# Performance work log

Hardware: AMD Instinct MI355X
Metric: run time of the kernel (lower is better)

Reference implementation:

```python
import jax, jax.numpy as jnp
import numpy as np

N = 50000
E = 800000
IN_C = 128
HEADS = 2
OUT_C = 64
NEG_SLOPE = 0.2  # PyG GATConv leaky_relu slope


def setup_inputs() -> dict:
    key = jax.random.key(0)
    ks = jax.random.split(key, 12)
    glorot = lambda k, shape: jax.random.normal(k, shape, jnp.float32) * np.sqrt(2.0 / (shape[0] + shape[-1]))
    return {
        "node_h": jax.random.normal(ks[0], (N, IN_C), jnp.float32),
        "edge_index_pc": jax.random.randint(ks[1], (2, E), 0, N, jnp.int64),
        "edge_index_mc": jax.random.randint(ks[2], (2, E), 0, N, jnp.int64),
        "W_pc": glorot(ks[3], (IN_C, HEADS * OUT_C)),
        "att_src_pc": glorot(ks[4], (HEADS, OUT_C)),
        "att_dst_pc": glorot(ks[5], (HEADS, OUT_C)),
        "bias_pc": jnp.zeros((HEADS * OUT_C,), jnp.float32),
        "W_mc": glorot(ks[6], (IN_C, HEADS * OUT_C)),
        "att_src_mc": glorot(ks[7], (HEADS, OUT_C)),
        "att_dst_mc": glorot(ks[8], (HEADS, OUT_C)),
        "bias_mc": jnp.zeros((HEADS * OUT_C,), jnp.float32),
    }


def _gat_conv(x, edge_index, W, att_src, att_dst, bias):
    # PyG GATConv (concat=True). x: [N, in], edge_index: [2, E] (src -> dst).
    n = x.shape[0]
    H, C = att_src.shape
    xw = (x @ W).reshape(n, H, C)                      # [N, H, C]
    a_src = jnp.sum(xw * att_src, axis=-1)             # [N, H]
    a_dst = jnp.sum(xw * att_dst, axis=-1)             # [N, H]
    src, dst = edge_index[0], edge_index[1]
    e = jax.nn.leaky_relu(a_src[src] + a_dst[dst], negative_slope=NEG_SLOPE)  # [E, H]
    # segment softmax over edges sharing the same destination node
    m = jax.ops.segment_max(e, dst, num_segments=n)    # [N, H]
    m = jnp.where(jnp.isfinite(m), m, 0.0)             # guard isolated nodes
    ex = jnp.exp(e - m[dst])
    denom = jax.ops.segment_sum(ex, dst, num_segments=n)
    alpha = ex / (denom[dst] + 1e-16)                  # [E, H]
    msg = xw[src] * alpha[:, :, None]                  # [E, H, C]
    out = jax.ops.segment_sum(msg, dst, num_segments=n)  # [N, H, C]
    return out.reshape(n, H * C) + bias


def reference(node_h, edge_index_pc, edge_index_mc,
              W_pc, att_src_pc, att_dst_pc, bias_pc,
              W_mc, att_src_mc, att_dst_mc, bias_mc):
    # eval mode: F.dropout and GATConv attention dropout are identity
    h_pc = jax.nn.elu(_gat_conv(node_h, edge_index_pc, W_pc, att_src_pc, att_dst_pc, bias_pc))
    h_mc = jax.nn.elu(_gat_conv(node_h, edge_index_mc, W_mc, att_src_mc, att_dst_mc, bias_mc))
    return (h_pc + h_mc) * 0.5
```

## Files before the change

### kernel.cpp

```cpp
#include <hip/hip_runtime.h>
#include <hip/hip_bf16.h>

#define IN_C   128
#define HC     128
#define OUT_C  64
#define EPB    4096
#define NBMAX  1024
#define CAP    4096

typedef short bf16x8 __attribute__((ext_vector_type(8)));
typedef float f32x4  __attribute__((ext_vector_type(4)));

__device__ __forceinline__ unsigned short f2bf(float f) {
    unsigned u = __float_as_uint(f);
    return (unsigned short)((u + 0x7FFF + ((u >> 16) & 1)) >> 16);
}

__device__ __forceinline__ void fma8(float* acc, float al, uint4 v) {
    acc[0] += al * __uint_as_float(v.x << 16);
    acc[1] += al * __uint_as_float(v.x & 0xFFFF0000u);
    acc[2] += al * __uint_as_float(v.y << 16);
    acc[3] += al * __uint_as_float(v.y & 0xFFFF0000u);
    acc[4] += al * __uint_as_float(v.z << 16);
    acc[5] += al * __uint_as_float(v.z & 0xFFFF0000u);
// ... 12 lines not shown
        for (int k = 0; k < 512; ++k) {
            int ex = (u[k] >> 7) & 0xFF;
            if (ex >= 0xE0) { f32 = 1; break; }
        }
        flags[0] = f32;
        const int* a = (const int*)e1;
        const int* b = (const int*)e2;
        int any1 = 0, any2 = 0;
        for (int k = 0; k < 64; ++k) { any1 |= a[2*k+1]; any2 |= b[2*k+1]; }
        flags[1] = (any1 == 0);
        flags[2] = (any2 == 0);
        flags[3] = 0;
    }
}

__device__ __forceinline__ float ldf(const void* p, int i, int f32) {
    if (f32) return ((const float*)p)[i];
    return __bfloat162float(((const __hip_bfloat16*)p)[i]);
}

__device__ __forceinline__ void load_edge(const void* ei, int e, int E, int i64,
                                          int& s, int& d)
{
    if (i64) {
        s = (int)((const long long*)ei)[e];
        d = (int)((const long long*)ei)[E + e];
    } else {
        s = ((const int*)ei)[e];
        d = ((const int*)ei)[E + e];
    }
}

__global__ void k_fill_sentinel(float* out, int total, float v)
{
    int i = blockIdx.x * blockDim.x + threadIdx.x;
    if (i < total) out[i] = v;
}

__global__ __launch_bounds__(256)
void k_prep(const void* __restrict__ Wpc, const void* __restrict__ Wmc,
            const int* __restrict__ flags,
            unsigned short* __restrict__ WTpc, unsigned short* __restrict__ WTmc)
{
    int idx = blockIdx.x * 256 + threadIdx.x;
    if (idx >= 2 * IN_C * HC) return;
    int conv = idx >= IN_C * HC;
    int r = idx - conv * IN_C * HC;
    int k = r >> 7, j = r & 127;
    float v = ldf(conv ? Wmc : Wpc, r, flags[0]);
    (conv ? WTmc : WTpc)[(size_t)j * IN_C + k] = f2bf(v);
}

__global__ __launch_bounds__(256)
void k_gemm_mfma2(const void* __restrict__ h,
                  const unsigned short* __restrict__ WT0,
                  const unsigned short* __restrict__ WT1,
                  const void* __restrict__ atS0, const void* __restrict__ atD0,
                  const void* __restrict__ atS1, const void* __restrict__ atD1,
                  const int* __restrict__ flags,
                  unsigned short* __restrict__ xw0, unsigned short* __restrict__ xw1,
                  float* __restrict__ oas0, float* __restrict__ oad0,
                  float* __restrict__ oas1, float* __restrict__ oad1,
                  int n)
{
    int conv = blockIdx.y;
    const unsigned short* WT = conv ? WT1 : WT0;
    const void* atS = conv ? atS1 : atS0;
    const void* atD = conv ? atD1 : atD0;
    unsigned short* xw = conv ? xw1 : xw0;
    float* oaS = conv ? oas1 : oas0;
    float* oaD = conv ? oad1 : oad0;

    int tid = threadIdx.x;
    int wave = tid >> 6, lane = tid & 63;
    int cl = lane & 15, grp = lane >> 4;
    int base = blockIdx.x * 64 + wave * 16;
    int f32 = flags[0];

    int nodeLoad = base + cl;
    int nl = nodeLoad < n ? nodeLoad : (n - 1);
    bf16x8 afr[4];
    #pragma unroll
    for (int s = 0; s < 4; ++s) {
        int k0 = 32 * s + 8 * grp;
        if (f32) {
            const float4* hr = (const float4*)((const float*)h + (size_t)nl * IN_C + k0);
            float4 u0 = hr[0], u1 = hr[1];
            afr[s][0] = (short)f2bf(u0.x); afr[s][1] = (short)f2bf(u0.y);
            afr[s][2] = (short)f2bf(u0.z); afr[s][3] = (short)f2bf(u0.w);
            afr[s][4] = (short)f2bf(u1.x); afr[s][5] = (short)f2bf(u1.y);
            afr[s][6] = (short)f2bf(u1.z); afr[s][7] = (short)f2bf(u1.w);
        } else {
            afr[s] = *(const bf16x8*)((const unsigned short*)h + (size_t)nl * IN_C + k0);
        }
    }

    float vs_[4][2] = {{0.f,0.f},{0.f,0.f},{0.f,0.f},{0.f,0.f}};
    float vd_[4][2] = {{0.f,0.f},{0.f,0.f},{0.f,0.f},{0.f,0.f}};

    #pragma unroll
    for (int t = 0; t < 8; ++t) {
        int col = t * 16 + cl;
        f32x4 acc = {0.f, 0.f, 0.f, 0.f};
        #pragma unroll
        for (int s = 0; s < 4; ++s) {
            int k0 = 32 * s + 8 * grp;
            bf16x8 b = *(const bf16x8*)(WT + (size_t)col * IN_C + k0);
            acc = __builtin_amdgcn_mfma_f32_16x16x32_bf16(afr[s], b, acc, 0, 0, 0);
        }
        float aS = ldf(atS, col, f32);
        float aD = ldf(atD, col, f32);
        int hd = t >> 2;
        #pragma unroll
        for (int r = 0; r < 4; ++r) {
            int nodeOut = base + 4 * grp + r;
            float v = acc[r];
            if (nodeOut < n) xw[(size_t)nodeOut * HC + col] = f2bf(v);
            vs_[r][hd] += v * aS;
            vd_[r][hd] += v * aD;
        }
    }
    #pragma unroll
    for (int r = 0; r < 4; ++r) {
        #pragma unroll
        for (int hd = 0; hd < 2; ++hd) {
            float vs = vs_[r][hd], vd = vd_[r][hd];
            #pragma unroll
            for (int off = 1; off < 16; off <<= 1) {
                vs += __shfl_xor(vs, off);
                vd += __shfl_xor(vd, off);
            }
            int nodeOut = base + 4 * grp + r;
            if (cl == 0 && nodeOut < n) {
                oaS[nodeOut * 2 + hd] = vs;
                oaD[nodeOut * 2 + hd] = vd;
            }
        }
    }
}

__global__ __launch_bounds__(256)
void k_bscatter3(const void* __restrict__ e1, const void* __restrict__ e2, int E,
                 const int* __restrict__ flags, int NB,
                 int* __restrict__ gcur1, int* __restrict__ gcur2,
                 unsigned* __restrict__ bkt1, unsigned* __restrict__ bkt2)
{
    __shared__ int cnt[NBMAX];
    __shared__ int lbase[NBMAX];
    int conv = blockIdx.y;
    const void* ei = conv ? e2 : e1;
    int* gcur = conv ? gcur2 : gcur1;
    unsigned* bkt = conv ? bkt2 : bkt1;
    int tid = threadIdx.x;
    for (int i = tid; i < NB; i += 256) cnt[i] = 0;
    __syncthreads();
    int base = blockIdx.x * EPB;
    int i64 = flags[1 + conv];
    int ss[EPB / 256], dd[EPB / 256];
    #pragma unroll
    for (int k = 0; k < EPB / 256; ++k) {
        int e = base + k * 256 + tid;
        if (e < E) {
            int s, d; load_edge(ei, e, E, i64, s, d);
            ss[k] = s; dd[k] = d;
            atomicAdd(&cnt[d >> 7], 1);
        } else dd[k] = -1;
    }
    __syncthreads();
    for (int i = tid; i < NB; i += 256) {
        int c = cnt[i];
        lbase[i] = c ? atomicAdd(&gcur[i], c) : 0;
        cnt[i] = 0;
    }
    __syncthreads();
    #pragma unroll
    for (int k = 0; k < EPB / 256; ++k) {
        if (dd[k] >= 0) {
            int b = dd[k] >> 7;
            int pos = lbase[b] + atomicAdd(&cnt[b], 1);
            if (pos < CAP)
                bkt[(size_t)b * CAP + pos] =
                    ((unsigned)(dd[k] & 127) << 17) | (unsigned)ss[k];
        }
    }
}

__global__ __launch_bounds__(256)
void k_bcsr3(unsigned* __restrict__ bkt1, unsigned* __restrict__ bkt2,
             const int* __restrict__ gcur1, const int* __restrict__ gcur2,
             int2* __restrict__ rs1, int2* __restrict__ rs2,
             int NB, int n)
{
    __shared__ unsigned ebuf[CAP];
    __shared__ int cnt[128], off[128], exc[128];
    int conv = blockIdx.y;
    unsigned* seg = (conv ? bkt2 : bkt1) + (size_t)blockIdx.x * CAP;
    const int* gcur = conv ? gcur2 : gcur1;
    int2* rs = conv ? rs2 : rs1;
    int b = blockIdx.x, tid = threadIdx.x;
    int nb0 = b << 7;
    int nd = n - nb0; if (nd > 128) nd = 128;
    int cntE = gcur[b]; if (cntE > CAP) cntE = CAP;

    for (int i = tid; i < cntE; i += 256) ebuf[i] = seg[i];
    if (tid < 128) cnt[tid] = 0;
    __syncthreads();
    for (int i = tid; i < cntE; i += 256)
        atomicAdd(&cnt[ebuf[i] >> 17], 1);
    __syncthreads();
    int v = (tid < 128) ? cnt[tid] : 0;
    if (tid < 128) off[tid] = v;
    __syncthreads();
    for (int o = 1; o < 128; o <<= 1) {
        int x = (tid < 128 && tid >= o) ? off[tid - o] : 0;
        __syncthreads();
        if (tid < 128) off[tid] += x;
        __syncthreads();
    }
    if (tid < 128) exc[tid] = off[tid] - v;
    if (tid < nd) {
        int begA = b * CAP + exc[tid];
        rs[nb0 + tid] = make_int2(begA, begA + v);
    }
    if (tid < 128) cnt[tid] = 0;
    __syncthreads();
    for (int i = tid; i < cntE; i += 256) {
        unsigned pv = ebuf[i];
        int d = pv >> 17;
        int pos = atomicAdd(&cnt[d], 1);
        seg[exc[d] + pos] = pv & 0x1FFFFu;
    }
}

__global__ __launch_bounds__(256)
void k_node8(const int2* __restrict__ rs1, const int2* __restrict__ rs2,
             const unsigned* __restrict__ csr1, const unsigned* __restrict__ csr2,
             const float* __restrict__ as1, const float* __restrict__ ad1,
             const float* __restrict__ as2, const float* __restrict__ ad2,
             const unsigned short* __restrict__ xw1, const unsigned short* __restrict__ xw2,
             const void* __restrict__ bias1, const void* __restrict__ bias2,
             const int* __restrict__ flags,
             float* __restrict__ out, int n)
{
    __shared__ int   slds[16][66];
    __shared__ float e0l[16][66];
    __shared__ float e1l[16][66];
    int tid = threadIdx.x;
    int nl = tid >> 4;
    int l  = tid & 15;
    int node = blockIdx.x * 16 + nl;
    if (node >= n) return;
    int f32 = flags[0];
    unsigned lofs = (unsigned)(l << 4);
    int c0 = l * 8;
    float vv0[8];

    #pragma unroll
    for (int conv = 0; conv < 2; ++conv) {
        const int2* rs = conv ? rs2 : rs1;
        const unsigned* csr = conv ? csr2 : csr1;
        const float2* asv = (const float2*)(conv ? as2 : as1);
        const float2* adv = (const float2*)(conv ? ad2 : ad1);
        const char* xwb = (const char*)(conv ? xw2 : xw1);
        const void* bias = conv ? bias2 : bias1;

        int2 r = rs[node];
        int beg = r.x, end = r.y;
        int deg = end - beg;
        float2 ad = adv[node];

        float m0 = -1e30f, m1 = -1e30f;
        for (int f = l; f < deg; f += 16) {
            int src = (int)csr[beg + f];
            float2 as = asv[src];
            float e0 = as.x + ad.x; e0 = e0 > 0.f ? e0 : 0.2f * e0;
            float e1 = as.y + ad.y; e1 = e1 > 0.f ? e1 : 0.2f * e1;
            if (f < 64) { slds[nl][f] = src; e0l[nl][f] = e0; e1l[nl][f] = e1; }
            m0 = fmaxf(m0, e0); m1 = fmaxf(m1, e1);
        }
        #pragma unroll
        for (int off = 8; off; off >>= 1) {
            m0 = fmaxf(m0, __shfl_xor(m0, off));
            m1 = fmaxf(m1, __shfl_xor(m1, off));
        }

        float s0 = 0.f, s1 = 0.f;
        for (int f = l; f < deg; f += 16) {
            float ex0, ex1;
            if (f < 64) {
                ex0 = expf(e0l[nl][f] - m0);
                ex1 = expf(e1l[nl][f] - m1);
                e0l[nl][f] = ex0; e1l[nl][f] = ex1;
            } else {
                int src = (int)csr[beg + f];
                float2 as = asv[src];
                float e0 = as.x + ad.x; e0 = e0 > 0.f ? e0 : 0.2f * e0;
                float e1 = as.y + ad.y; e1 = e1 > 0.f ? e1 : 0.2f * e1;
                ex0 = expf(e0 - m0); ex1 = expf(e1 - m1);
            }
            s0 += ex0; s1 += ex1;
        }
        #pragma unroll
        for (int off = 8; off; off >>= 1) {
            s0 += __shfl_xor(s0, off);
            s1 += __shfl_xor(s1, off);
        }
        float inv = (l < 8) ? 1.f / (s0 + 1e-16f) : 1.f / (s1 + 1e-16f);
        float mh  = (l < 8) ? m0 : m1;

        float acc[8] = {0.f,0.f,0.f,0.f,0.f,0.f,0.f,0.f};
        int tcap = deg < 64 ? deg : 64;
        int t = 0;
        for (; t + 4 <= tcap; t += 4) {
            int sA = slds[nl][t],   sB = slds[nl][t+1];
            int sC = slds[nl][t+2], sD = slds[nl][t+3];
            float aA = (l < 8) ? e0l[nl][t]   : e1l[nl][t];
            float aB = (l < 8) ? e0l[nl][t+1] : e1l[nl][t+1];
            float aC = (l < 8) ? e0l[nl][t+2] : e1l[nl][t+2];
            float aD = (l < 8) ? e0l[nl][t+3] : e1l[nl][t+3];
            uint4 vA = *(const uint4*)(xwb + (((unsigned)sA) << 8) + lofs);
            uint4 vB = *(const uint4*)(xwb + (((unsigned)sB) << 8) + lofs);
            uint4 vC = *(const uint4*)(xwb + (((unsigned)sC) << 8) + lofs);
            uint4 vD = *(const uint4*)(xwb + (((unsigned)sD) << 8) + lofs);
            fma8(acc, aA * inv, vA);
            fma8(acc, aB * inv, vB);
            fma8(acc, aC * inv, vC);
            fma8(acc, aD * inv, vD);
        }
        for (; t < tcap; ++t) {
            int src = slds[nl][t];
            float exv = (l < 8) ? e0l[nl][t] : e1l[nl][t];
            uint4 v = *(const uint4*)(xwb + (((unsigned)src) << 8) + lofs);
            fma8(acc, exv * inv, v);
        }
        for (; t < deg; ++t) {
            int src = (int)csr[beg + t];
            float2 as = asv[src];
            float e = (l < 8) ? (as.x + ad.x) : (as.y + ad.y);
            e = e > 0.f ? e : 0.2f * e;
            float exv = expf(e - mh);
            uint4 v = *(const uint4*)(xwb + (((unsigned)src) << 8) + lofs);
            fma8(acc, exv * inv, v);
        }

        if (conv == 0) {
            #pragma unroll
            for (int j = 0; j < 8; ++j) {
                float v = acc[j] + ldf(bias, c0 + j, f32);
                vv0[j] = v > 0.f ? v : expf(v) - 1.f;
            }
        } else {
            float vv1[8];
            #pragma unroll
            for (int j = 0; j < 8; ++j) {
                float v = acc[j] + ldf(bias, c0 + j, f32);
                vv1[j] = v > 0.f ? v : expf(v) - 1.f;
            }
            float4* o4 = (float4*)(out + (size_t)node * HC + c0);
            o4[0] = make_float4(0.5f * (vv0[0] + vv1[0]), 0.5f * (vv0[1] + vv1[1]),
                                0.5f * (vv0[2] + vv1[2]), 0.5f * (vv0[3] + vv1[3]));
            o4[1] = make_float4(0.5f * (vv0[4] + vv1[4]), 0.5f * (vv0[5] + vv1[5]),
                                0.5f * (vv0[6] + vv1[6]), 0.5f * (vv0[7] + vv1[7]));
        }
    }
}

static inline char* align64(char* p) {
    return (char*)(((size_t)p + 63) & ~(size_t)63);
}

extern "C" void kernel_launch(void* const* d_in, const int* in_sizes, int n_in,
                              void* d_out, int out_size, void* d_ws, size_t ws_size,
                              hipStream_t stream)
{
    const void* node_h = d_in[0];
    const void* ei_pc  = d_in[1];
    const void* ei_mc  = d_in[2];
    const void* W_pc   = d_in[3];
    const void* as_pc  = d_in[4];
    const void* ad_pc  = d_in[5];
    const void* b_pc   = d_in[6];
    const void* W_mc   = d_in[7];
    const void* as_mc  = d_in[8];
    const void* ad_mc  = d_in[9];
    const void* b_mc   = d_in[10];

    const int N = in_sizes[0] / IN_C;
    const int E = in_sizes[1] / 2;
    const int total = N * HC;
    const int NB = (N + 127) >> 7;
    float* out = (float*)d_out;
    const int fillBlocks = (out_size + 255) / 256;

    char* p = (char*)d_ws;
    int* flags = (int*)p;                       p += 256;
    unsigned short* WT_pc = (unsigned short*)p; p += (size_t)IN_C * HC * 2;
    unsigned short* WT_mc = (unsigned short*)p; p += (size_t)IN_C * HC * 2;
    unsigned short* xw_pc = (unsigned short*)p; p += (size_t)total * 2;
    unsigned short* xw_mc = (unsigned short*)p; p += (size_t)total * 2;
    float* aspc = (float*)p;                    p += (size_t)N * 2 * 4;
    float* adpc = (float*)p;                    p += (size_t)N * 2 * 4;
    float* asmc = (float*)p;                    p += (size_t)N * 2 * 4;
    float* admc = (float*)p;                    p += (size_t)N * 2 * 4;
    char* zbase = p;
    int* gcur1 = (int*)p;                       p += (size_t)NBMAX * 4;
    int* gcur2 = (int*)p;                       p += (size_t)NBMAX * 4;
    size_t zbytes = (size_t)(p - zbase);
    p = align64(p);
    int2* rs1 = (int2*)p;                       p += (size_t)N * 8;  p = align64(p);
    int2* rs2 = (int2*)p;                       p += (size_t)N * 8;  p = align64(p);
    unsigned* bkt1 = (unsigned*)p;              p += (size_t)NB * CAP * 4;
    unsigned* bkt2 = (unsigned*)p;              p += (size_t)NB * CAP * 4;

    {
        float sentinel = 0.f;
        if (n_in < 11) sentinel = 690.f;
        else if (in_sizes[1] != in_sizes[2]) sentinel = 702.f;
        else if (in_sizes[3] != IN_C * HC)   sentinel = 703.f;
        else if (in_sizes[7] != IN_C * HC)   sentinel = 707.f;
        else if (out_size != total)          sentinel = 720.f;
        else if (NB > NBMAX)                 sentinel = 730.f;
        else if (N >= (1 << 17))             sentinel = 741.f;
        size_t need = (size_t)(p - (char*)d_ws);
        if (sentinel == 0.f && ws_size < need) sentinel = 555.f;
        if (sentinel != 0.f) {
            k_fill_sentinel<<<fillBlocks, 256, 0, stream>>>(out, out_size, sentinel);
            return;
        }
    }

    k_detect<<<1, 64, 0, stream>>>(node_h, ei_pc, ei_mc, flags);
    k_prep<<<(2 * IN_C * HC + 255) / 256, 256, 0, stream>>>(W_pc, W_mc, flags, WT_pc, WT_mc);
    hipMemsetAsync(zbase, 0, zbytes, stream);

    const int blocksB = (E + EPB - 1) / EPB;
    const int blocksN = (N + 15) / 16;
    const int blocksG = (N + 63) / 64;

    k_gemm_mfma2<<<dim3(blocksG, 2), 256, 0, stream>>>(node_h, WT_pc, WT_mc,
                                                       as_pc, ad_pc, as_mc, ad_mc, flags,
                                                       xw_pc, xw_mc, aspc, adpc, asmc, admc, N);

    k_bscatter3<<<dim3(blocksB, 2), 256, 0, stream>>>(ei_pc, ei_mc, E, flags, NB,
                                                      gcur1, gcur2, bkt1, bkt2);
    k_bcsr3<<<dim3(NB, 2), 256, 0, stream>>>(bkt1, bkt2, gcur1, gcur2, rs1, rs2, NB, N);

    k_node8<<<blocksN, 256, 0, stream>>>(rs1, rs2, bkt1, bkt2,
                                         aspc, adpc, asmc, admc,
                                         xw_pc, xw_mc, b_pc, b_mc, flags,
                                         out, N);
}
```

Measured before the change: 156.9 us.

## Merge GEMM and edge bucket scatter into one launch; interleave both convs in aggregation

```diff
diff --git a/kernel.cpp b/kernel.cpp
--- a/kernel.cpp
+++ b/kernel.cpp
@@ -88,135 +88,137 @@
 }
 
 __global__ __launch_bounds__(256)
-void k_gemm_mfma2(const void* __restrict__ h,
-                  const unsigned short* __restrict__ WT0,
-                  const unsigned short* __restrict__ WT1,
-                  const void* __restrict__ atS0, const void* __restrict__ atD0,
-                  const void* __restrict__ atS1, const void* __restrict__ atD1,
-                  const int* __restrict__ flags,
-                  unsigned short* __restrict__ xw0, unsigned short* __restrict__ xw1,
-                  float* __restrict__ oas0, float* __restrict__ oad0,
-                  float* __restrict__ oas1, float* __restrict__ oad1,
-                  int n)
-{
-    int conv = blockIdx.y;
-    const unsigned short* WT = conv ? WT1 : WT0;
-    const void* atS = conv ? atS1 : atS0;
-    const void* atD = conv ? atD1 : atD0;
-    unsigned short* xw = conv ? xw1 : xw0;
-    float* oaS = conv ? oas1 : oas0;
-    float* oaD = conv ? oad1 : oad0;
-
+void k_gs(const void* __restrict__ h,
+          const unsigned short* __restrict__ WT0,
+          const unsigned short* __restrict__ WT1,
+          const void* __restrict__ atS0, const void* __restrict__ atD0,
+          const void* __restrict__ atS1, const void* __restrict__ atD1,
+          const int* __restrict__ flags,
+          unsigned short* __restrict__ xw0, unsigned short* __restrict__ xw1,
+          float* __restrict__ oas0, float* __restrict__ oad0,
+          float* __restrict__ oas1, float* __restrict__ oad1,
+          int n, int blocksG,
+          const void* __restrict__ e1, const void* __restrict__ e2, int E,
+          int NB, int blocksB,
+          int* __restrict__ gcur1, int* __restrict__ gcur2,
+          unsigned* __restrict__ bkt1, unsigned* __restrict__ bkt2)
+{
+    __shared__ int sh[2 * NBMAX];
     int tid = threadIdx.x;
-    int wave = tid >> 6, lane = tid & 63;
-    int cl = lane & 15, grp = lane >> 4;
-    int base = blockIdx.x * 64 + wave * 16;
-    int f32 = flags[0];
-
-    int nodeLoad = base + cl;
-    int nl = nodeLoad < n ? nodeLoad : (n - 1);
-    bf16x8 afr[4];
-    #pragma unroll
-    for (int s = 0; s < 4; ++s) {
-        int k0 = 32 * s + 8 * grp;
-        if (f32) {
-            const float4* hr = (const float4*)((const float*)h + (size_t)nl * IN_C + k0);
-            float4 u0 = hr[0], u1 = hr[1];
-            afr[s][0] = (short)f2bf(u0.x); afr[s][1] = (short)f2bf(u0.y);
-            afr[s][2] = (short)f2bf(u0.z); afr[s][3] = (short)f2bf(u0.w);
-            afr[s][4] = (short)f2bf(u1.x); afr[s][5] = (short)f2bf(u1.y);
-            afr[s][6] = (short)f2bf(u1.z); afr[s][7] = (short)f2bf(u1.w);
-        } else {
-            afr[s] = *(const bf16x8*)((const unsigned short*)h + (size_t)nl * IN_C + k0);
-        }
-    }
-
-    float vs_[4][2] = {{0.f,0.f},{0.f,0.f},{0.f,0.f},{0.f,0.f}};
-    float vd_[4][2] = {{0.f,0.f},{0.f,0.f},{0.f,0.f},{0.f,0.f}};
-
-    #pragma unroll
-    for (int t = 0; t < 8; ++t) {
-        int col = t * 16 + cl;
-        f32x4 acc = {0.f, 0.f, 0.f, 0.f};
+
+    if (blockIdx.y < 2) {
+        if ((int)blockIdx.x >= blocksG) return;
+        int conv = blockIdx.y;
+        const unsigned short* WT = conv ? WT1 : WT0;
+        const void* atS = conv ? atS1 : atS0;
+        const void* atD = conv ? atD1 : atD0;
+        unsigned short* xw = conv ? xw1 : xw0;
+        float* oaS = conv ? oas1 : oas0;
+        float* oaD = conv ? oad1 : oad0;
+
+        int wave = tid >> 6, lane = tid & 63;
+        int cl = lane & 15, grp = lane >> 4;
+        int base = blockIdx.x * 64 + wave * 16;
+        int f32 = flags[0];
+
+        int nodeLoad = base + cl;
+        int nl = nodeLoad < n ? nodeLoad : (n - 1);
+        bf16x8 afr[4];
         #pragma unroll
         for (int s = 0; s < 4; ++s) {
             int k0 = 32 * s + 8 * grp;
-            bf16x8 b = *(const bf16x8*)(WT + (size_t)col * IN_C + k0);
-            acc = __builtin_amdgcn_mfma_f32_16x16x32_bf16(afr[s], b, acc, 0, 0, 0);
-        }
-        float aS = ldf(atS, col, f32);
-        float aD = ldf(atD, col, f32);
-        int hd = t >> 2;
+            if (f32) {
+                const float4* hr = (const float4*)((const float*)h + (size_t)nl * IN_C + k0);
+                float4 u0 = hr[0], u1 = hr[1];
+                afr[s][0] = (short)f2bf(u0.x); afr[s][1] = (short)f2bf(u0.y);
+                afr[s][2] = (short)f2bf(u0.z); afr[s][3] = (short)f2bf(u0.w);
+                afr[s][4] = (short)f2bf(u1.x); afr[s][5] = (short)f2bf(u1.y);
+                afr[s][6] = (short)f2bf(u1.z); afr[s][7] = (short)f2bf(u1.w);
+            } else {
+                afr[s] = *(const bf16x8*)((const unsigned short*)h + (size_t)nl * IN_C + k0);
+            }
+        }
+
+        float vs_[4][2] = {{0.f,0.f},{0.f,0.f},{0.f,0.f},{0.f,0.f}};
+        float vd_[4][2] = {{0.f,0.f},{0.f,0.f},{0.f,0.f},{0.f,0.f}};
+
+        #pragma unroll
+        for (int t = 0; t < 8; ++t) {
+            int col = t * 16 + cl;
+            f32x4 acc = {0.f, 0.f, 0.f, 0.f};
+            #pragma unroll
+            for (int s = 0; s < 4; ++s) {
+                int k0 = 32 * s + 8 * grp;
+                bf16x8 b = *(const bf16x8*)(WT + (size_t)col * IN_C + k0);
+                acc = __builtin_amdgcn_mfma_f32_16x16x32_bf16(afr[s], b, acc, 0, 0, 0);
+            }
+            float aS = ldf(atS, col, f32);
+            float aD = ldf(atD, col, f32);
+            int hd = t >> 2;
+            #pragma unroll
+            for (int r = 0; r < 4; ++r) {
+                int nodeOut = base + 4 * grp + r;
+                float v = acc[r];
+                if (nodeOut < n) xw[(size_t)nodeOut * HC + col] = f2bf(v);
+                vs_[r][hd] += v * aS;
+                vd_[r][hd] += v * aD;
+            }
+        }
         #pragma unroll
         for (int r = 0; r < 4; ++r) {
-            int nodeOut = base + 4 * grp + r;
-            float v = acc[r];
-            if (nodeOut < n) xw[(size_t)nodeOut * HC + col] = f2bf(v);
-            vs_[r][hd] += v * aS;
-            vd_[r][hd] += v * aD;
-        }
-    }
-    #pragma unroll
-    for (int r = 0; r < 4; ++r) {
+            #pragma unroll
+            for (int hd = 0; hd < 2; ++hd) {
+                float vs = vs_[r][hd], vd = vd_[r][hd];
+                #pragma unroll
+                for (int off = 1; off < 16; off <<= 1) {
+                    vs += __shfl_xor(vs, off);
+                    vd += __shfl_xor(vd, off);
+                }
+                int nodeOut = base + 4 * grp + r;
+                if (cl == 0 && nodeOut < n) {
+                    oaS[nodeOut * 2 + hd] = vs;
+                    oaD[nodeOut * 2 + hd] = vd;
+                }
+            }
+        }
+    } else {
+        if ((int)blockIdx.x >= blocksB) return;
+        int conv = blockIdx.y - 2;
+        const void* ei = conv ? e2 : e1;
+        int* gcur = conv ? gcur2 : gcur1;
+        unsigned* bkt = conv ? bkt2 : bkt1;
+        int* cnt = sh;
+        int* lbase = sh + NBMAX;
+        for (int i = tid; i < NB; i += 256) cnt[i] = 0;
+        __syncthreads();
+        int base = blockIdx.x * EPB;
+        int i64 = flags[1 + conv];
+        int ss[EPB / 256], dd[EPB / 256];
         #pragma unroll
-        for (int hd = 0; hd < 2; ++hd) {
-            float vs = vs_[r][hd], vd = vd_[r][hd];
-            #pragma unroll
-            for (int off = 1; off < 16; off <<= 1) {
-                vs += __shfl_xor(vs, off);
-                vd += __shfl_xor(vd, off);
+        for (int k = 0; k < EPB / 256; ++k) {
+            int e = base + k * 256 + tid;
+            if (e < E) {
+                int s, d; load_edge(ei, e, E, i64, s, d);
+                ss[k] = s; dd[k] = d;
+                atomicAdd(&cnt[d >> 7], 1);
+            } else dd[k] = -1;
+        }
+        __syncthreads();
+        for (int i = tid; i < NB; i += 256) {
+            int c = cnt[i];
+            lbase[i] = c ? atomicAdd(&gcur[i], c) : 0;
+            cnt[i] = 0;
+        }
+        __syncthreads();
+        #pragma unroll
+        for (int k = 0; k < EPB / 256; ++k) {
+            if (dd[k] >= 0) {
+                int b = dd[k] >> 7;
+                int pos = lbase[b] + atomicAdd(&cnt[b], 1);
+                if (pos < CAP)
+                    bkt[(size_t)b * CAP + pos] =
+                        ((unsigned)(dd[k] & 127) << 17) | (unsigned)ss[k];
             }
-            int nodeOut = base + 4 * grp + r;
-            if (cl == 0 && nodeOut < n) {
-                oaS[nodeOut * 2 + hd] = vs;
-                oaD[nodeOut * 2 + hd] = vd;
-            }
-        }
-    }
-}
-
-__global__ __launch_bounds__(256)
-void k_bscatter3(const void* __restrict__ e1, const void* __restrict__ e2, int E,
-                 const int* __restrict__ flags, int NB,
-                 int* __restrict__ gcur1, int* __restrict__ gcur2,
-                 unsigned* __restrict__ bkt1, unsigned* __restrict__ bkt2)
-{
-    __shared__ int cnt[NBMAX];
-    __shared__ int lbase[NBMAX];
-    int conv = blockIdx.y;
-    const void* ei = conv ? e2 : e1;
-    int* gcur = conv ? gcur2 : gcur1;
-    unsigned* bkt = conv ? bkt2 : bkt1;
-    int tid = threadIdx.x;
-    for (int i = tid; i < NB; i += 256) cnt[i] = 0;
-    __syncthreads();
-    int base = blockIdx.x * EPB;
-    int i64 = flags[1 + conv];
-    int ss[EPB / 256], dd[EPB / 256];
-    #pragma unroll
-    for (int k = 0; k < EPB / 256; ++k) {
-        int e = base + k * 256 + tid;
-        if (e < E) {
-            int s, d; load_edge(ei, e, E, i64, s, d);
-            ss[k] = s; dd[k] = d;
-            atomicAdd(&cnt[d >> 7], 1);
-        } else dd[k] = -1;
-    }
-    __syncthreads();
-    for (int i = tid; i < NB; i += 256) {
-        int c = cnt[i];
-        lbase[i] = c ? atomicAdd(&gcur[i], c) : 0;
-        cnt[i] = 0;
-    }
-    __syncthreads();
-    #pragma unroll
-    for (int k = 0; k < EPB / 256; ++k) {
-        if (dd[k] >= 0) {
-            int b = dd[k] >> 7;
-            int pos = lbase[b] + atomicAdd(&cnt[b], 1);
-            if (pos < CAP)
-                bkt[(size_t)b * CAP + pos] =
-                    ((unsigned)(dd[k] & 127) << 17) | (unsigned)ss[k];
         }
     }
 }
@@ -269,7 +271,7 @@
 }
 
 __global__ __launch_bounds__(256)
-void k_node8(const int2* __restrict__ rs1, const int2* __restrict__ rs2,
+void k_node9(const int2* __restrict__ rs1, const int2* __restrict__ rs2,
              const unsigned* __restrict__ csr1, const unsigned* __restrict__ csr2,
              const float* __restrict__ as1, const float* __restrict__ ad1,
              const float* __restrict__ as2, const float* __restrict__ ad2,
@@ -278,9 +280,9 @@
              const int* __restrict__ flags,
              float* __restrict__ out, int n)
 {
-    __shared__ int   slds[16][66];
-    __shared__ float e0l[16][66];
-    __shared__ float e1l[16][66];
+    __shared__ int   slds0[16][66], slds1[16][66];
+    __shared__ float e0l0[16][66], e1l0[16][66];
+    __shared__ float e0l1[16][66], e1l1[16][66];
     int tid = threadIdx.x;
     int nl = tid >> 4;
     int l  = tid & 15;
@@ -289,116 +291,193 @@
     int f32 = flags[0];
     unsigned lofs = (unsigned)(l << 4);
     int c0 = l * 8;
-    float vv0[8];
-
+
+    const float2* asv0 = (const float2*)as1;
+    const float2* adv0 = (const float2*)ad1;
+    const float2* asv1 = (const float2*)as2;
+    const float2* adv1 = (const float2*)ad2;
+    const char* xb0 = (const char*)xw1;
+    const char* xb1 = (const char*)xw2;
+
+    int2 r0 = rs1[node], r1 = rs2[node];
+    int beg0 = r0.x, deg0 = r0.y - r0.x;
+    int beg1 = r1.x, deg1 = r1.y - r1.x;
+    float2 ad0 = adv0[node], ad1v = adv1[node];
+
+    float m00 = -1e30f, m10 = -1e30f;
+    for (int f = l; f < deg0; f += 16) {
+        int src = (int)csr1[beg0 + f];
+        float2 as = asv0[src];
+        float e0 = as.x + ad0.x; e0 = e0 > 0.f ? e0 : 0.2f * e0;
+        float e1 = as.y + ad0.y; e1 = e1 > 0.f ? e1 : 0.2f * e1;
+        if (f < 64) { slds0[nl][f] = src; e0l0[nl][f] = e0; e1l0[nl][f] = e1; }
+        m00 = fmaxf(m00, e0); m10 = fmaxf(m10, e1);
+    }
+    float m01 = -1e30f, m11 = -1e30f;
+    for (int f = l; f < deg1; f += 16) {
+        int src = (int)csr2[beg1 + f];
+        float2 as = asv1[src];
+        float e0 = as.x + ad1v.x; e0 = e0 > 0.f ? e0 : 0.2f * e0;
+        float e1 = as.y + ad1v.y; e1 = e1 > 0.f ? e1 : 0.2f * e1;
+        if (f < 64) { slds1[nl][f] = src; e0l1[nl][f] = e0; e1l1[nl][f] = e1; }
+        m01 = fmaxf(m01, e0); m11 = fmaxf(m11, e1);
+    }
     #pragma unroll
-    for (int conv = 0; conv < 2; ++conv) {
-        const int2* rs = conv ? rs2 : rs1;
-        const unsigned* csr = conv ? csr2 : csr1;
-        const float2* asv = (const float2*)(conv ? as2 : as1);
-        const float2* adv = (const float2*)(conv ? ad2 : ad1);
-        const char* xwb = (const char*)(conv ? xw2 : xw1);
-        const void* bias = conv ? bias2 : bias1;
-
-        int2 r = rs[node];
-        int beg = r.x, end = r.y;
-        int deg = end - beg;
-        float2 ad = adv[node];
-
-        float m0 = -1e30f, m1 = -1e30f;
-        for (int f = l; f < deg; f += 16) {
-            int src = (int)csr[beg + f];
-            float2 as = asv[src];
-            float e0 = as.x + ad.x; e0 = e0 > 0.f ? e0 : 0.2f * e0;
-            float e1 = as.y + ad.y; e1 = e1 > 0.f ? e1 : 0.2f * e1;
-            if (f < 64) { slds[nl][f] = src; e0l[nl][f] = e0; e1l[nl][f] = e1; }
-            m0 = fmaxf(m0, e0); m1 = fmaxf(m1, e1);
-        }
-        #pragma unroll
-        for (int off = 8; off; off >>= 1) {
-            m0 = fmaxf(m0, __shfl_xor(m0, off));
-            m1 = fmaxf(m1, __shfl_xor(m1, off));
-        }
-
-        float s0 = 0.f, s1 = 0.f;
-        for (int f = l; f < deg; f += 16) {
-            float ex0, ex1;
-            if (f < 64) {
-                ex0 = expf(e0l[nl][f] - m0);
-                ex1 = expf(e1l[nl][f] - m1);
-                e0l[nl][f] = ex0; e1l[nl][f] = ex1;
-            } else {
-                int src = (int)csr[beg + f];
-                float2 as = asv[src];
-                float e0 = as.x + ad.x; e0 = e0 > 0.f ? e0 : 0.2f * e0;
-                float e1 = as.y + ad.y; e1 = e1 > 0.f ? e1 : 0.2f * e1;
-                ex0 = expf(e0 - m0); ex1 = expf(e1 - m1);
-            }
-            s0 += ex0; s1 += ex1;
-        }
-        #pragma unroll
-        for (int off = 8; off; off >>= 1) {
-            s0 += __shfl_xor(s0, off);
-            s1 += __shfl_xor(s1, off);
-        }
-        float inv = (l < 8) ? 1.f / (s0 + 1e-16f) : 1.f / (s1 + 1e-16f);
-        float mh  = (l < 8) ? m0 : m1;
-
-        float acc[8] = {0.f,0.f,0.f,0.f,0.f,0.f,0.f,0.f};
-        int tcap = deg < 64 ? deg : 64;
-        int t = 0;
-        for (; t + 4 <= tcap; t += 4) {
-            int sA = slds[nl][t],   sB = slds[nl][t+1];
-            int sC = slds[nl][t+2], sD = slds[nl][t+3];
-            float aA = (l < 8) ? e0l[nl][t]   : e1l[nl][t];
-            float aB = (l < 8) ? e0l[nl][t+1] : e1l[nl][t+1];
-            float aC = (l < 8) ? e0l[nl][t+2] : e1l[nl][t+2];
-            float aD = (l < 8) ? e0l[nl][t+3] : e1l[nl][t+3];
-            uint4 vA = *(const uint4*)(xwb + (((unsigned)sA) << 8) + lofs);
-            uint4 vB = *(const uint4*)(xwb + (((unsigned)sB) << 8) + lofs);
-            uint4 vC = *(const uint4*)(xwb + (((unsigned)sC) << 8) + lofs);
-            uint4 vD = *(const uint4*)(xwb + (((unsigned)sD) << 8) + lofs);
-            fma8(acc, aA * inv, vA);
-            fma8(acc, aB * inv, vB);
-            fma8(acc, aC * inv, vC);
-            fma8(acc, aD * inv, vD);
-        }
-        for (; t < tcap; ++t) {
-            int src = slds[nl][t];
-            float exv = (l < 8) ? e0l[nl][t] : e1l[nl][t];
-            uint4 v = *(const uint4*)(xwb + (((unsigned)src) << 8) + lofs);
-            fma8(acc, exv * inv, v);
-        }
-        for (; t < deg; ++t) {
-            int src = (int)csr[beg + t];
-            float2 as = asv[src];
-            float e = (l < 8) ? (as.x + ad.x) : (as.y + ad.y);
-            e = e > 0.f ? e : 0.2f * e;
-            float exv = expf(e - mh);
-            uint4 v = *(const uint4*)(xwb + (((unsigned)src) << 8) + lofs);
-            fma8(acc, exv * inv, v);
-        }
-
-        if (conv == 0) {
-            #pragma unroll
-            for (int j = 0; j < 8; ++j) {
-                float v = acc[j] + ldf(bias, c0 + j, f32);
-                vv0[j] = v > 0.f ? v : expf(v) - 1.f;
-            }
+    for (int off = 8; off; off >>= 1) {
+        m00 = fmaxf(m00, __shfl_xor(m00, off));
+        m10 = fmaxf(m10, __shfl_xor(m10, off));
+        m01 = fmaxf(m01, __shfl_xor(m01, off));
+        m11 = fmaxf(m11, __shfl_xor(m11, off));
+    }
+
+    float s00 = 0.f, s10 = 0.f;
+    for (int f = l; f < deg0; f += 16) {
+        float ex0, ex1;
+        if (f < 64) {
+            ex0 = expf(e0l0[nl][f] - m00);
+            ex1 = expf(e1l0[nl][f] - m10);
+            e0l0[nl][f] = ex0; e1l0[nl][f] = ex1;
         } else {
-            float vv1[8];
-            #pragma unroll
-            for (int j = 0; j < 8; ++j) {
-                float v = acc[j] + ldf(bias, c0 + j, f32);
-                vv1[j] = v > 0.f ? v : expf(v) - 1.f;
-            }
-            float4* o4 = (float4*)(out + (size_t)node * HC + c0);
-            o4[0] = make_float4(0.5f * (vv0[0] + vv1[0]), 0.5f * (vv0[1] + vv1[1]),
-                                0.5f * (vv0[2] + vv1[2]), 0.5f * (vv0[3] + vv1[3]));
-            o4[1] = make_float4(0.5f * (vv0[4] + vv1[4]), 0.5f * (vv0[5] + vv1[5]),
-                                0.5f * (vv0[6] + vv1[6]), 0.5f * (vv0[7] + vv1[7]));
-        }
-    }
+            int src = (int)csr1[beg0 + f];
+            float2 as = asv0[src];
+            float e0 = as.x + ad0.x; e0 = e0 > 0.f ? e0 : 0.2f * e0;
+            float e1 = as.y + ad0.y; e1 = e1 > 0.f ? e1 : 0.2f * e1;
+            ex0 = expf(e0 - m00); ex1 = expf(e1 - m10);
+        }
+        s00 += ex0; s10 += ex1;
+    }
+    float s01 = 0.f, s11 = 0.f;
+    for (int f = l; f < deg1; f += 16) {
+        float ex0, ex1;
+        if (f < 64) {
+            ex0 = expf(e0l1[nl][f] - m01);
+            ex1 = expf(e1l1[nl][f] - m11);
+            e0l1[nl][f] = ex0; e1l1[nl][f] = ex1;
+        } else {
+            int src = (int)csr2[beg1 + f];
+            float2 as = asv1[src];
+            float e0 = as.x + ad1v.x; e0 = e0 > 0.f ? e0 : 0.2f * e0;
+            float e1 = as.y + ad1v.y; e1 = e1 > 0.f ? e1 : 0.2f * e1;
+            ex0 = expf(e0 - m01); ex1 = expf(e1 - m11);
+        }
+        s01 += ex0; s11 += ex1;
+    }
+    #pragma unroll
+    for (int off = 8; off; off >>= 1) {
+        s00 += __shfl_xor(s00, off);
+        s10 += __shfl_xor(s10, off);
+        s01 += __shfl_xor(s01, off);
+        s11 += __shfl_xor(s11, off);
+    }
+    float inv_0 = (l < 8) ? 1.f / (s00 + 1e-16f) : 1.f / (s10 + 1e-16f);
+    float inv_1 = (l < 8) ? 1.f / (s01 + 1e-16f) : 1.f / (s11 + 1e-16f);
+    float mh0 = (l < 8) ? m00 : m10;
+    float mh1 = (l < 8) ? m01 : m11;
+
+    float acc0[8] = {0,0,0,0,0,0,0,0};
+    float acc1[8] = {0,0,0,0,0,0,0,0};
+    int tc0 = deg0 < 64 ? deg0 : 64;
+    int tc1 = deg1 < 64 ? deg1 : 64;
+    int t0 = 0, t1 = 0;
+    while (t0 + 4 <= tc0 && t1 + 4 <= tc1) {
+        int a0 = slds0[nl][t0],   a1 = slds0[nl][t0+1];
+        int a2 = slds0[nl][t0+2], a3 = slds0[nl][t0+3];
+        int b0 = slds1[nl][t1],   b1 = slds1[nl][t1+1];
+        int b2 = slds1[nl][t1+2], b3 = slds1[nl][t1+3];
+        uint4 vA = *(const uint4*)(xb0 + (((unsigned)a0) << 8) + lofs);
+        uint4 vB = *(const uint4*)(xb0 + (((unsigned)a1) << 8) + lofs);
+        uint4 vC = *(const uint4*)(xb0 + (((unsigned)a2) << 8) + lofs);
+        uint4 vD = *(const uint4*)(xb0 + (((unsigned)a3) << 8) + lofs);
+        uint4 wA = *(const uint4*)(xb1 + (((unsigned)b0) << 8) + lofs);
+        uint4 wB = *(const uint4*)(xb1 + (((unsigned)b1) << 8) + lofs);
+        uint4 wC = *(const uint4*)(xb1 + (((unsigned)b2) << 8) + lofs);
+        uint4 wD = *(const uint4*)(xb1 + (((unsigned)b3) << 8) + lofs);
+        float pA = ((l < 8) ? e0l0[nl][t0]   : e1l0[nl][t0])   * inv_0;
+        float pB = ((l < 8) ? e0l0[nl][t0+1] : e1l0[nl][t0+1]) * inv_0;
+        float pC = ((l < 8) ? e0l0[nl][t0+2] : e1l0[nl][t0+2]) * inv_0;
+        float pD = ((l < 8) ? e0l0[nl][t0+3] : e1l0[nl][t0+3]) * inv_0;
+        float qA = ((l < 8) ? e0l1[nl][t1]   : e1l1[nl][t1])   * inv_1;
+        float qB = ((l < 8) ? e0l1[nl][t1+1] : e1l1[nl][t1+1]) * inv_1;
+        float qC = ((l < 8) ? e0l1[nl][t1+2] : e1l1[nl][t1+2]) * inv_1;
+        float qD = ((l < 8) ? e0l1[nl][t1+3] : e1l1[nl][t1+3]) * inv_1;
+        fma8(acc0, pA, vA); fma8(acc0, pB, vB);
+        fma8(acc0, pC, vC); fma8(acc0, pD, vD);
+        fma8(acc1, qA, wA); fma8(acc1, qB, wB);
+        fma8(acc1, qC, wC); fma8(acc1, qD, wD);
+        t0 += 4; t1 += 4;
+    }
+    for (; t0 + 4 <= tc0; t0 += 4) {
+        int a0 = slds0[nl][t0],   a1 = slds0[nl][t0+1];
+        int a2 = slds0[nl][t0+2], a3 = slds0[nl][t0+3];
+        uint4 vA = *(const uint4*)(xb0 + (((unsigned)a0) << 8) + lofs);
+        uint4 vB = *(const uint4*)(xb0 + (((unsigned)a1) << 8) + lofs);
+        uint4 vC = *(const uint4*)(xb0 + (((unsigned)a2) << 8) + lofs);
+        uint4 vD = *(const uint4*)(xb0 + (((unsigned)a3) << 8) + lofs);
+        float pA = ((l < 8) ? e0l0[nl][t0]   : e1l0[nl][t0])   * inv_0;
+        float pB = ((l < 8) ? e0l0[nl][t0+1] : e1l0[nl][t0+1]) * inv_0;
+        float pC = ((l < 8) ? e0l0[nl][t0+2] : e1l0[nl][t0+2]) * inv_0;
+        float pD = ((l < 8) ? e0l0[nl][t0+3] : e1l0[nl][t0+3]) * inv_0;
+        fma8(acc0, pA, vA); fma8(acc0, pB, vB);
+        fma8(acc0, pC, vC); fma8(acc0, pD, vD);
+    }
+    for (; t1 + 4 <= tc1; t1 += 4) {
+        int b0 = slds1[nl][t1],   b1 = slds1[nl][t1+1];
+        int b2 = slds1[nl][t1+2], b3 = slds1[nl][t1+3];
+        uint4 wA = *(const uint4*)(xb1 + (((unsigned)b0) << 8) + lofs);
+        uint4 wB = *(const uint4*)(xb1 + (((unsigned)b1) << 8) + lofs);
+        uint4 wC = *(const uint4*)(xb1 + (((unsigned)b2) << 8) + lofs);
+        uint4 wD = *(const uint4*)(xb1 + (((unsigned)b3) << 8) + lofs);
+        float qA = ((l < 8) ? e0l1[nl][t1]   : e1l1[nl][t1])   * inv_1;
+        float qB = ((l < 8) ? e0l1[nl][t1+1] : e1l1[nl][t1+1]) * inv_1;
+        float qC = ((l < 8) ? e0l1[nl][t1+2] : e1l1[nl][t1+2]) * inv_1;
+        float qD = ((l < 8) ? e0l1[nl][t1+3] : e1l1[nl][t1+3]) * inv_1;
+        fma8(acc1, qA, wA); fma8(acc1, qB, wB);
+        fma8(acc1, qC, wC); fma8(acc1, qD, wD);
+    }
+    for (; t0 < tc0; ++t0) {
+        int src = slds0[nl][t0];
+        float p = ((l < 8) ? e0l0[nl][t0] : e1l0[nl][t0]) * inv_0;
+        uint4 v = *(const uint4*)(xb0 + (((unsigned)src) << 8) + lofs);
+        fma8(acc0, p, v);
+    }
+    for (; t1 < tc1; ++t1) {
+        int src = slds1[nl][t1];
+        float q = ((l < 8) ? e0l1[nl][t1] : e1l1[nl][t1]) * inv_1;
+        uint4 v = *(const uint4*)(xb1 + (((unsigned)src) << 8) + lofs);
+        fma8(acc1, q, v);
+    }
+    for (; t0 < deg0; ++t0) {
+        int src = (int)csr1[beg0 + t0];
+        float2 as = asv0[src];
+        float e = (l < 8) ? (as.x + ad0.x) : (as.y + ad0.y);
+        e = e > 0.f ? e : 0.2f * e;
+        uint4 v = *(const uint4*)(xb0 + (((unsigned)src) << 8) + lofs);
+        fma8(acc0, expf(e - mh0) * inv_0, v);
+    }
+    for (; t1 < deg1; ++t1) {
+        int src = (int)csr2[beg1 + t1];
+        float2 as = asv1[src];
+        float e = (l < 8) ? (as.x + ad1v.x) : (as.y + ad1v.y);
+        e = e > 0.f ? e : 0.2f * e;
+        uint4 v = *(const uint4*)(xb1 + (((unsigned)src) << 8) + lofs);
+        fma8(acc1, expf(e - mh1) * inv_1, v);
+    }
+
+    float4 o0, o1;
+    float r_[8];
+    #pragma unroll
+    for (int j = 0; j < 8; ++j) {
+        float v0 = acc0[j] + ldf(bias1, c0 + j, f32);
+        float v1 = acc1[j] + ldf(bias2, c0 + j, f32);
+        v0 = v0 > 0.f ? v0 : expf(v0) - 1.f;
+        v1 = v1 > 0.f ? v1 : expf(v1) - 1.f;
+        r_[j] = 0.5f * (v0 + v1);
+    }
+    o0 = make_float4(r_[0], r_[1], r_[2], r_[3]);
+    o1 = make_float4(r_[4], r_[5], r_[6], r_[7]);
+    float4* o4 = (float4*)(out + (size_t)node * HC + c0);
+    o4[0] = o0;
+    o4[1] = o1;
 }
 
 static inline char* align64(char* p) {
@@ -472,16 +551,18 @@
     const int blocksB = (E + EPB - 1) / EPB;
     const int blocksN = (N + 15) / 16;
     const int blocksG = (N + 63) / 64;
-
-    k_gemm_mfma2<<<dim3(blocksG, 2), 256, 0, stream>>>(node_h, WT_pc, WT_mc,
-                                                       as_pc, ad_pc, as_mc, ad_mc, flags,
-                                                       xw_pc, xw_mc, aspc, adpc, asmc, admc, N);
-
-    k_bscatter3<<<dim3(blocksB, 2), 256, 0, stream>>>(ei_pc, ei_mc, E, flags, NB,
-                                                      gcur1, gcur2, bkt1, bkt2);
+    const int gx = blocksG > blocksB ? blocksG : blocksB;
+
+    k_gs<<<dim3(gx, 4), 256, 0, stream>>>(node_h, WT_pc, WT_mc,
+                                          as_pc, ad_pc, as_mc, ad_mc, flags,
+                                          xw_pc, xw_mc, aspc, adpc, asmc, admc,
+                                          N, blocksG,
+                                          ei_pc, ei_mc, E, NB, blocksB,
+                                          gcur1, gcur2, bkt1, bkt2);
+
     k_bcsr3<<<dim3(NB, 2), 256, 0, stream>>>(bkt1, bkt2, gcur1, gcur2, rs1, rs2, NB, N);
 
-    k_node8<<<blocksN, 256, 0, stream>>>(rs1, rs2, bkt1, bkt2,
+    k_node9<<<blocksN, 256, 0, stream>>>(rs1, rs2, bkt1, bkt2,
                                          aspc, adpc, asmc, admc,
                                          xw_pc, xw_mc, b_pc, b_mc, flags,
                                          out, N);
```

Measured after the change: 159.7 us. Within noise of the previous version (+1.7%).

## Fuse GEMM and edge bucket scatter into one launch; unroll gather by 8

Applied to the files above, without the earlier changes.

```diff
diff --git a/kernel.cpp b/kernel.cpp
--- a/kernel.cpp
+++ b/kernel.cpp
@@ -88,135 +88,137 @@
 }
 
 __global__ __launch_bounds__(256)
-void k_gemm_mfma2(const void* __restrict__ h,
-                  const unsigned short* __restrict__ WT0,
-                  const unsigned short* __restrict__ WT1,
-                  const void* __restrict__ atS0, const void* __restrict__ atD0,
-                  const void* __restrict__ atS1, const void* __restrict__ atD1,
-                  const int* __restrict__ flags,
-                  unsigned short* __restrict__ xw0, unsigned short* __restrict__ xw1,
-                  float* __restrict__ oas0, float* __restrict__ oad0,
-                  float* __restrict__ oas1, float* __restrict__ oad1,
-                  int n)
-{
-    int conv = blockIdx.y;
-    const unsigned short* WT = conv ? WT1 : WT0;
-    const void* atS = conv ? atS1 : atS0;
-    const void* atD = conv ? atD1 : atD0;
-    unsigned short* xw = conv ? xw1 : xw0;
-    float* oaS = conv ? oas1 : oas0;
-    float* oaD = conv ? oad1 : oad0;
-
+void k_gs(const void* __restrict__ h,
+          const unsigned short* __restrict__ WT0,
+          const unsigned short* __restrict__ WT1,
+          const void* __restrict__ atS0, const void* __restrict__ atD0,
+          const void* __restrict__ atS1, const void* __restrict__ atD1,
+          const int* __restrict__ flags,
+          unsigned short* __restrict__ xw0, unsigned short* __restrict__ xw1,
+          float* __restrict__ oas0, float* __restrict__ oad0,
+          float* __restrict__ oas1, float* __restrict__ oad1,
+          int n, int blocksG,
+          const void* __restrict__ e1, const void* __restrict__ e2, int E,
+          int NB, int blocksB,
+          int* __restrict__ gcur1, int* __restrict__ gcur2,
+          unsigned* __restrict__ bkt1, unsigned* __restrict__ bkt2)
+{
+    __shared__ int sh[2 * NBMAX];
     int tid = threadIdx.x;
-    int wave = tid >> 6, lane = tid & 63;
-    int cl = lane & 15, grp = lane >> 4;
-    int base = blockIdx.x * 64 + wave * 16;
-    int f32 = flags[0];
-
-    int nodeLoad = base + cl;
-    int nl = nodeLoad < n ? nodeLoad : (n - 1);
-    bf16x8 afr[4];
-    #pragma unroll
-    for (int s = 0; s < 4; ++s) {
-        int k0 = 32 * s + 8 * grp;
-        if (f32) {
-            const float4* hr = (const float4*)((const float*)h + (size_t)nl * IN_C + k0);
-            float4 u0 = hr[0], u1 = hr[1];
-            afr[s][0] = (short)f2bf(u0.x); afr[s][1] = (short)f2bf(u0.y);
-            afr[s][2] = (short)f2bf(u0.z); afr[s][3] = (short)f2bf(u0.w);
-            afr[s][4] = (short)f2bf(u1.x); afr[s][5] = (short)f2bf(u1.y);
-            afr[s][6] = (short)f2bf(u1.z); afr[s][7] = (short)f2bf(u1.w);
-        } else {
-            afr[s] = *(const bf16x8*)((const unsigned short*)h + (size_t)nl * IN_C + k0);
-        }
-    }
-
-    float vs_[4][2] = {{0.f,0.f},{0.f,0.f},{0.f,0.f},{0.f,0.f}};
-    float vd_[4][2] = {{0.f,0.f},{0.f,0.f},{0.f,0.f},{0.f,0.f}};
-
-    #pragma unroll
-    for (int t = 0; t < 8; ++t) {
-        int col = t * 16 + cl;
-        f32x4 acc = {0.f, 0.f, 0.f, 0.f};
+
+    if (blockIdx.y < 2) {
+        if ((int)blockIdx.x >= blocksG) return;
+        int conv = blockIdx.y;
+        const unsigned short* WT = conv ? WT1 : WT0;
+        const void* atS = conv ? atS1 : atS0;
+        const void* atD = conv ? atD1 : atD0;
+        unsigned short* xw = conv ? xw1 : xw0;
+        float* oaS = conv ? oas1 : oas0;
+        float* oaD = conv ? oad1 : oad0;
+
+        int wave = tid >> 6, lane = tid & 63;
+        int cl = lane & 15, grp = lane >> 4;
+        int base = blockIdx.x * 64 + wave * 16;
+        int f32 = flags[0];
+
+        int nodeLoad = base + cl;
+        int nl = nodeLoad < n ? nodeLoad : (n - 1);
+        bf16x8 afr[4];
         #pragma unroll
         for (int s = 0; s < 4; ++s) {
             int k0 = 32 * s + 8 * grp;
-            bf16x8 b = *(const bf16x8*)(WT + (size_t)col * IN_C + k0);
-            acc = __builtin_amdgcn_mfma_f32_16x16x32_bf16(afr[s], b, acc, 0, 0, 0);
-        }
-        float aS = ldf(atS, col, f32);
-        float aD = ldf(atD, col, f32);
-        int hd = t >> 2;
+            if (f32) {
+                const float4* hr = (const float4*)((const float*)h + (size_t)nl * IN_C + k0);
+                float4 u0 = hr[0], u1 = hr[1];
+                afr[s][0] = (short)f2bf(u0.x); afr[s][1] = (short)f2bf(u0.y);
+                afr[s][2] = (short)f2bf(u0.z); afr[s][3] = (short)f2bf(u0.w);
+                afr[s][4] = (short)f2bf(u1.x); afr[s][5] = (short)f2bf(u1.y);
+                afr[s][6] = (short)f2bf(u1.z); afr[s][7] = (short)f2bf(u1.w);
+            } else {
+                afr[s] = *(const bf16x8*)((const unsigned short*)h + (size_t)nl * IN_C + k0);
+            }
+        }
+
+        float vs_[4][2] = {{0.f,0.f},{0.f,0.f},{0.f,0.f},{0.f,0.f}};
+        float vd_[4][2] = {{0.f,0.f},{0.f,0.f},{0.f,0.f},{0.f,0.f}};
+
+        #pragma unroll
+        for (int t = 0; t < 8; ++t) {
+            int col = t * 16 + cl;
+            f32x4 acc = {0.f, 0.f, 0.f, 0.f};
+            #pragma unroll
+            for (int s = 0; s < 4; ++s) {
+                int k0 = 32 * s + 8 * grp;
+                bf16x8 b = *(const bf16x8*)(WT + (size_t)col * IN_C + k0);
+                acc = __builtin_amdgcn_mfma_f32_16x16x32_bf16(afr[s], b, acc, 0, 0, 0);
+            }
+            float aS = ldf(atS, col, f32);
+            float aD = ldf(atD, col, f32);
+            int hd = t >> 2;
+            #pragma unroll
+            for (int r = 0; r < 4; ++r) {
+                int nodeOut = base + 4 * grp + r;
+                float v = acc[r];
+                if (nodeOut < n) xw[(size_t)nodeOut * HC + col] = f2bf(v);
+                vs_[r][hd] += v * aS;
+                vd_[r][hd] += v * aD;
+            }
+        }
         #pragma unroll
         for (int r = 0; r < 4; ++r) {
-            int nodeOut = base + 4 * grp + r;
-            float v = acc[r];
-            if (nodeOut < n) xw[(size_t)nodeOut * HC + col] = f2bf(v);
-            vs_[r][hd] += v * aS;
-            vd_[r][hd] += v * aD;
-        }
-    }
-    #pragma unroll
-    for (int r = 0; r < 4; ++r) {
-        #pragma unroll
-        for (int hd = 0; hd < 2; ++hd) {
-            float vs = vs_[r][hd], vd = vd_[r][hd];
             #pragma unroll
-            for (int off = 1; off < 16; off <<= 1) {
-                vs += __shfl_xor(vs, off);
-                vd += __shfl_xor(vd, off);
-            }
-            int nodeOut = base + 4 * grp + r;
-            if (cl == 0 && nodeOut < n) {
-                oaS[nodeOut * 2 + hd] = vs;
-                oaD[nodeOut * 2 + hd] = vd;
-            }
-        }
-    }
-}
-
-__global__ __launch_bounds__(256)
-void k_bscatter3(const void* __restrict__ e1, const void* __restrict__ e2, int E,
-                 const int* __restrict__ flags, int NB,
-                 int* __restrict__ gcur1, int* __restrict__ gcur2,
-                 unsigned* __restrict__ bkt1, unsigned* __restrict__ bkt2)
-{
-    __shared__ int cnt[NBMAX];
-    __shared__ int lbase[NBMAX];
-    int conv = blockIdx.y;
-    const void* ei = conv ? e2 : e1;
-    int* gcur = conv ? gcur2 : gcur1;
-    unsigned* bkt = conv ? bkt2 : bkt1;
-    int tid = threadIdx.x;
-    for (int i = tid; i < NB; i += 256) cnt[i] = 0;
-    __syncthreads();
-    int base = blockIdx.x * EPB;
-    int i64 = flags[1 + conv];
-    int ss[EPB / 256], dd[EPB / 256];
-    #pragma unroll
-    for (int k = 0; k < EPB / 256; ++k) {
-        int e = base + k * 256 + tid;
-        if (e < E) {
-            int s, d; load_edge(ei, e, E, i64, s, d);
-            ss[k] = s; dd[k] = d;
-            atomicAdd(&cnt[d >> 7], 1);
-        } else dd[k] = -1;
-    }
-    __syncthreads();
-    for (int i = tid; i < NB; i += 256) {
-        int c = cnt[i];
-        lbase[i] = c ? atomicAdd(&gcur[i], c) : 0;
-        cnt[i] = 0;
-    }
-    __syncthreads();
-    #pragma unroll
-    for (int k = 0; k < EPB / 256; ++k) {
-        if (dd[k] >= 0) {
-            int b = dd[k] >> 7;
-            int pos = lbase[b] + atomicAdd(&cnt[b], 1);
-            if (pos < CAP)
-                bkt[(size_t)b * CAP + pos] =
-                    ((unsigned)(dd[k] & 127) << 17) | (unsigned)ss[k];
+            for (int hd = 0; hd < 2; ++hd) {
+                float vs = vs_[r][hd], vd = vd_[r][hd];
+                #pragma unroll
+                for (int off = 1; off < 16; off <<= 1) {
+                    vs += __shfl_xor(vs, off);
+                    vd += __shfl_xor(vd, off);
+                }
+                int nodeOut = base + 4 * grp + r;
+                if (cl == 0 && nodeOut < n) {
+                    oaS[nodeOut * 2 + hd] = vs;
+                    oaD[nodeOut * 2 + hd] = vd;
+                }
+            }
+        }
+    } else {
+        if ((int)blockIdx.x >= blocksB) return;
+        int conv = blockIdx.y - 2;
+        const void* ei = conv ? e2 : e1;
+        int* gcur = conv ? gcur2 : gcur1;
+        unsigned* bkt = conv ? bkt2 : bkt1;
+        int* cnt = sh;
+        int* lbase = sh + NBMAX;
+        for (int i = tid; i < NB; i += 256) cnt[i] = 0;
+        __syncthreads();
+        int base = blockIdx.x * EPB;
+        int i64 = flags[1 + conv];
+        int ss[EPB / 256], dd[EPB / 256];
+        #pragma unroll
+        for (int k = 0; k < EPB / 256; ++k) {
+            int e = base + k * 256 + tid;
+            if (e < E) {
+                int s, d; load_edge(ei, e, E, i64, s, d);
+                ss[k] = s; dd[k] = d;
+                atomicAdd(&cnt[d >> 7], 1);
+            } else dd[k] = -1;
+        }
+        __syncthreads();
+        for (int i = tid; i < NB; i += 256) {
+            int c = cnt[i];
+            lbase[i] = c ? atomicAdd(&gcur[i], c) : 0;
+            cnt[i] = 0;
+        }
+        __syncthreads();
+        #pragma unroll
+        for (int k = 0; k < EPB / 256; ++k) {
+            if (dd[k] >= 0) {
+                int b = dd[k] >> 7;
+                int pos = lbase[b] + atomicAdd(&cnt[b], 1);
+                if (pos < CAP)
+                    bkt[(size_t)b * CAP + pos] =
+                        ((unsigned)(dd[k] & 127) << 17) | (unsigned)ss[k];
+            }
         }
     }
 }
@@ -347,27 +349,47 @@
         float acc[8] = {0.f,0.f,0.f,0.f,0.f,0.f,0.f,0.f};
         int tcap = deg < 64 ? deg : 64;
         int t = 0;
+        for (; t + 8 <= tcap; t += 8) {
+            int s_[8]; float a_[8];
+            #pragma unroll
+            for (int u = 0; u < 8; ++u) {
+                s_[u] = slds[nl][t + u];
+                a_[u] = ((l < 8) ? e0l[nl][t + u] : e1l[nl][t + u]) * inv;
+            }
+            uint4 v0 = *(const uint4*)(xwb + (((unsigned)s_[0]) << 8) + lofs);
+            uint4 v1 = *(const uint4*)(xwb + (((unsigned)s_[1]) << 8) + lofs);
+            uint4 v2 = *(const uint4*)(xwb + (((unsigned)s_[2]) << 8) + lofs);
+            uint4 v3 = *(const uint4*)(xwb + (((unsigned)s_[3]) << 8) + lofs);
+            uint4 v4 = *(const uint4*)(xwb + (((unsigned)s_[4]) << 8) + lofs);
+            uint4 v5 = *(const uint4*)(xwb + (((unsigned)s_[5]) << 8) + lofs);
+            uint4 v6 = *(const uint4*)(xwb + (((unsigned)s_[6]) << 8) + lofs);
+            uint4 v7 = *(const uint4*)(xwb + (((unsigned)s_[7]) << 8) + lofs);
+            fma8(acc, a_[0], v0); fma8(acc, a_[1], v1);
+            fma8(acc, a_[2], v2); fma8(acc, a_[3], v3);
+            fma8(acc, a_[4], v4); fma8(acc, a_[5], v5);
+            fma8(acc, a_[6], v6); fma8(acc, a_[7], v7);
+        }
         for (; t + 4 <= tcap; t += 4) {
             int sA = slds[nl][t],   sB = slds[nl][t+1];
             int sC = slds[nl][t+2], sD = slds[nl][t+3];
-            float aA = (l < 8) ? e0l[nl][t]   : e1l[nl][t];
-            float aB = (l < 8) ? e0l[nl][t+1] : e1l[nl][t+1];
-            float aC = (l < 8) ? e0l[nl][t+2] : e1l[nl][t+2];
-            float aD = (l < 8) ? e0l[nl][t+3] : e1l[nl][t+3];
+            float aA = ((l < 8) ? e0l[nl][t]   : e1l[nl][t])   * inv;
+            float aB = ((l < 8) ? e0l[nl][t+1] : e1l[nl][t+1]) * inv;
+            float aC = ((l < 8) ? e0l[nl][t+2] : e1l[nl][t+2]) * inv;
+            float aD = ((l < 8) ? e0l[nl][t+3] : e1l[nl][t+3]) * inv;
             uint4 vA = *(const uint4*)(xwb + (((unsigned)sA) << 8) + lofs);
             uint4 vB = *(const uint4*)(xwb + (((unsigned)sB) << 8) + lofs);
             uint4 vC = *(const uint4*)(xwb + (((unsigned)sC) << 8) + lofs);
             uint4 vD = *(const uint4*)(xwb + (((unsigned)sD) << 8) + lofs);
-            fma8(acc, aA * inv, vA);
-            fma8(acc, aB * inv, vB);
-            fma8(acc, aC * inv, vC);
-            fma8(acc, aD * inv, vD);
+            fma8(acc, aA, vA);
+            fma8(acc, aB, vB);
+            fma8(acc, aC, vC);
+            fma8(acc, aD, vD);
         }
         for (; t < tcap; ++t) {
             int src = slds[nl][t];
-            float exv = (l < 8) ? e0l[nl][t] : e1l[nl][t];
+            float exv = ((l < 8) ? e0l[nl][t] : e1l[nl][t]) * inv;
             uint4 v = *(const uint4*)(xwb + (((unsigned)src) << 8) + lofs);
-            fma8(acc, exv * inv, v);
+            fma8(acc, exv, v);
         }
         for (; t < deg; ++t) {
             int src = (int)csr[beg + t];
@@ -472,13 +494,15 @@
     const int blocksB = (E + EPB - 1) / EPB;
     const int blocksN = (N + 15) / 16;
     const int blocksG = (N + 63) / 64;
-
-    k_gemm_mfma2<<<dim3(blocksG, 2), 256, 0, stream>>>(node_h, WT_pc, WT_mc,
-                                                       as_pc, ad_pc, as_mc, ad_mc, flags,
-                                                       xw_pc, xw_mc, aspc, adpc, asmc, admc, N);
-
-    k_bscatter3<<<dim3(blocksB, 2), 256, 0, stream>>>(ei_pc, ei_mc, E, flags, NB,
-                                                      gcur1, gcur2, bkt1, bkt2);
+    const int gx = blocksG > blocksB ? blocksG : blocksB;
+
+    k_gs<<<dim3(gx, 4), 256, 0, stream>>>(node_h, WT_pc, WT_mc,
+                                          as_pc, ad_pc, as_mc, ad_mc, flags,
+                                          xw_pc, xw_mc, aspc, adpc, asmc, admc,
+                                          N, blocksG,
+                                          ei_pc, ei_mc, E, NB, blocksB,
+                                          gcur1, gcur2, bkt1, bkt2);
+
     k_bcsr3<<<dim3(NB, 2), 256, 0, stream>>>(bkt1, bkt2, gcur1, gcur2, rs1, rs2, NB, N);
 
     k_node8<<<blocksN, 256, 0, stream>>>(rs1, rs2, bkt1, bkt2,
```

Measured after the change: 149.6 us. 4.7% less time.
